# Kernel tuning notes

Measured on AMD Instinct MI355X. Metric: run time of the kernel, lower is better.

Reference implementation:

```python
import jax, jax.numpy as jnp
import numpy as np
from functools import partial

POOL_H, POOL_W = 7, 7


def _bin_index(coord, start, stop, step, n_bins):
    """Map each pixel coordinate to its ROI-pool bin index (or n_bins if outside ROI).

    Bins i < n_bins-1 span [start + i*step, start + (i+1)*step); the last bin
    extends to `stop` (matching the original `(i+1)*h_step if i+1<pool_h else region_h`).
    coord: [L]; start/stop/step: [R] int32. Returns [R, L] int32 in [0, n_bins].
    """
    rel = coord[None, :] - start[:, None]                      # [R, L]
    idx = jnp.minimum(rel // jnp.maximum(step, 1)[:, None], n_bins - 1)
    idx = jnp.where(step[:, None] > 0, idx, n_bins - 1)        # step==0 -> all pixels in last bin
    valid = (rel >= 0) & (coord[None, :] < stop[:, None])
    return jnp.where(valid, idx, n_bins).astype(jnp.int32)


def _roi_pool_image(fm, rois, ph, pw):
    """fm: [H, W, C], rois: [R, 4] relative (h0, w0, h1, w1). Returns [R, ph, pw, C]."""
    H, W, C = fm.shape
    h0 = (H * rois[:, 0]).astype(jnp.int32)   # truncation == tf.cast(..., int32) for >=0
    w0 = (W * rois[:, 1]).astype(jnp.int32)
    h1 = (H * rois[:, 2]).astype(jnp.int32)
    w1 = (W * rois[:, 3]).astype(jnp.int32)
    h_step = (h1 - h0) // ph
    w_step = (w1 - w0) // pw

    idx_h = _bin_index(jnp.arange(H), h0, h1, h_step, ph)      # [R, H]
    idx_w = _bin_index(jnp.arange(W), w0, w1, w_step, pw)      # [R, W]

    neg = jnp.finfo(fm.dtype).min
    fm_whc = jnp.swapaxes(fm, 0, 1)                            # [W, H, C]

    def pool_one(ih, iw):
        # scatter-max columns into width bins (extra slot pw collects out-of-ROI pixels)
        t = jnp.full((pw + 1, H, C), neg, fm.dtype).at[iw].max(fm_whc)[:pw]  # [pw, H, C]
        # scatter-max rows into height bins
        o = jnp.full((ph + 1, pw, C), neg, fm.dtype).at[ih].max(jnp.swapaxes(t, 0, 1))[:ph]
        return o                                               # [ph, pw, C]

    return jax.vmap(pool_one)(idx_h, idx_w)


def setup_inputs() -> dict:
    key = jax.random.key(0)
    k1, k2, k3 = jax.random.split(key, 3)
    feature_map = jax.random.normal(k1, (2, 64, 64, 256), dtype=jnp.float32)
    starts = jax.random.uniform(k2, (2, 256, 2), minval=0.0, maxval=0.3)
    ends = jax.random.uniform(k3, (2, 256, 2), minval=0.6, maxval=1.0)
    rois = jnp.concatenate([starts, ends], axis=-1).astype(jnp.float32)  # (h0, w0, h1, w1)
    return {"feature_map": feature_map, "rois": rois}


def reference(feature_map, rois):
    # per-image ROI max pooling, vmapped over the batch -> [B, R, ph, pw, C]
    pool = partial(_roi_pool_image, ph=POOL_H, pw=POOL_W)
    return jax.vmap(pool)(feature_map, rois)
```

## Files before the change

### kernel.cpp

```cpp
#include <hip/hip_runtime.h>
#include <float.h>

constexpr int H = 64, W = 64, C = 256, PH = 7, PW = 7;

typedef float f32x4 __attribute__((ext_vector_type(4)));

__device__ __forceinline__ f32x4 vmax4(f32x4 a, f32x4 b) {
    f32x4 r;
    r.x = fmaxf(a.x, b.x); r.y = fmaxf(a.y, b.y);
    r.z = fmaxf(a.z, b.z); r.w = fmaxf(a.w, b.w);
    return r;
}

__global__ __launch_bounds__(256) void build_tables(
    const float* __restrict__ fm, float* __restrict__ s4x,
    float* __restrict__ s4y, float* __restrict__ s4xy)
{
    __shared__ f32x4 lds_fm[7][64];
    __shared__ f32x4 lds_sx[7][64];

    const int lane = threadIdx.x & 63;
    const int wave = __builtin_amdgcn_readfirstlane(threadIdx.x >> 6);

    const int x8 = blockIdx.x & 7;
    const int z  = blockIdx.x >> 3;
    const int b  = x8 >> 2;
    const int quart = x8 & 3;
    const int x  = z & (W - 1);
    const int y0 = quart * 16 + ((z >> 6) << 2);

    const int x1 = min(x + 1, W - 1), x2 = min(x + 2, W - 1), x3 = min(x + 3, W - 1);
    const float* fmb = fm + (size_t)b * H * W * C + (size_t)lane * 4;

    #pragma unroll
    for (int s = 0; s < 2; ++s) {
        const int slot = wave + 4 * s;
        if (slot < 7) {
            const int y = min(y0 + slot, H - 1);
            const float* row = fmb + (size_t)y * W * C;
            f32x4 v0 = *(const f32x4*)(row + (size_t)x  * C);
            f32x4 v1 = *(const f32x4*)(row + (size_t)x1 * C);
            f32x4 v2 = *(const f32x4*)(row + (size_t)x2 * C);
            f32x4 v3 = *(const f32x4*)(row + (size_t)x3 * C);
            lds_fm[slot][lane] = v0;
            lds_sx[slot][lane] = vmax4(vmax4(v0, v1), vmax4(v2, v3));
        }
    }
    __syncthreads();

    const int y = y0 + wave;
    const f32x4 sx = lds_sx[wave][lane];
    const f32x4 sy = vmax4(vmax4(lds_fm[wave][lane],     lds_fm[wave + 1][lane]),
                           vmax4(lds_fm[wave + 2][lane], lds_fm[wave + 3][lane]));
    const f32x4 sxy = vmax4(vmax4(lds_sx[wave][lane],     lds_sx[wave + 1][lane]),
                            vmax4(lds_sx[wave + 2][lane], lds_sx[wave + 3][lane]));

    const size_t o = ((size_t)(b * H + y) * W + x) * C + (size_t)lane * 4;
    *(f32x4*)(s4x  + o) = sx;
    *(f32x4*)(s4y  + o) = sy;
    *(f32x4*)(s4xy + o) = sxy;
}

__global__ __launch_bounds__(256) void roi_pool_q(
    const float* __restrict__ fm, const float* __restrict__ rois,
    const float* __restrict__ s4x, const float* __restrict__ s4y,
    const float* __restrict__ s4xy, float* __restrict__ out, int R)
{
    const int lane = threadIdx.x & 63;
    const int wave = __builtin_amdgcn_readfirstlane(threadIdx.x >> 6);

    const int x8 = blockIdx.x & 7;
    const int n  = blockIdx.x >> 3;
    const int b  = x8 >> 2;
    const int g  = x8 & 3;

    int i, id;
    if (g < 3) {
        i  = 2 * g + (n & 1);
        id = (n >> 1) * 4 + wave;
    } else {
        if (n >= 448) return;
        i  = 6;
        id = n * 4 + wave;
    }
    const int r = id / 7;
    const int j = id - 7 * r;

    const float* roi = rois + ((size_t)b * R + r) * 4;
    int h0 = (int)((float)H * roi[0]);
    int w0 = (int)((float)W * roi[1]);
    int h1 = (int)((float)H * roi[2]);
    int w1 = (int)((float)W * roi[3]);
    int hs = (h1 - h0) / PH;
    int ws = (w1 - w0) / PW;

    int ys, ye, xs, xe;
    if (hs > 0) { ys = h0 + i * hs; ye = (i < PH - 1) ? (ys + hs) : h1; }
    else        { ys = h0;          ye = (i == PH - 1) ? h1 : h0; }
    if (ws > 0) { xs = w0 + j * ws; xe = (j < PW - 1) ? (xs + ws) : w1; }
    else        { xs = w0;          xe = (j == PW - 1) ? w1 : w0; }
    ys = __builtin_amdgcn_readfirstlane(max(ys, 0));
    ye = __builtin_amdgcn_readfirstlane(min(ye, H));
    xs = __builtin_amdgcn_readfirstlane(max(xs, 0));
    xe = __builtin_amdgcn_readfirstlane(min(xe, W));

    const int hl = ye - ys, wl = xe - xs;
    const f32x4 NEG = {-FLT_MAX, -FLT_MAX, -FLT_MAX, -FLT_MAX};
    f32x4 a0 = NEG, a1 = NEG, a2 = NEG, a3 = NEG;

    if (hl > 0 && wl > 0) {
        const bool y4 = hl >= 4, x4 = wl >= 4;
        const int ny = y4 ? (hl + 3) >> 2 : hl;
        const int nx = x4 ? (wl + 3) >> 2 : wl;
        const int ystep = y4 ? 4 : 1, xstep = x4 ? 4 : 1;
        const int ycl = y4 ? ye - 4 : ye - 1;
        const int xcl = x4 ? xe - 4 : xe - 1;
        const float* tb = y4 ? (x4 ? s4xy : s4y) : (x4 ? s4x : fm);
        const float* tbb = tb + (size_t)b * H * W * C + lane * 4;

        const int xo0 = min(xs,             xcl) * C;
        const int xo1 = min(xs + xstep,     xcl) * C;
        const int xo2 = min(xs + 2 * xstep, xcl) * C;
        const int xo3 = min(xs + 3 * xstep, xcl) * C;

        #pragma unroll
        for (int ky = 0; ky < 4; ++ky) {
            if (ky < ny) {
                const int y = min(ys + ystep * ky, ycl);
                const float* rowp = tbb + (size_t)y * (W * C);
                a0 = vmax4(a0, *(const f32x4*)(rowp + xo0));
                if (nx > 1) a1 = vmax4(a1, *(const f32x4*)(rowp + xo1));
                if (nx > 2) a2 = vmax4(a2, *(const f32x4*)(rowp + xo2));
                if (nx > 3) a3 = vmax4(a3, *(const f32x4*)(rowp + xo3));
            }
        }
    }
    const f32x4 acc = vmax4(vmax4(a0, a1), vmax4(a2, a3));

    size_t o = ((((size_t)b * R + r) * PH + i) * PW + j) * C + (size_t)lane * 4;
    __builtin_nontemporal_store(acc, reinterpret_cast<f32x4*>(out + o));
}

__global__ __launch_bounds__(256) void roi_pool_direct(
    const float* __restrict__ fm, const float* __restrict__ rois,
    float* __restrict__ out, int R)
{
    const int lane = threadIdx.x & 63;
    const int wave = __builtin_amdgcn_readfirstlane(threadIdx.x >> 6);
    const int b = blockIdx.x & 1;
    int m = (blockIdx.x >> 1) * 4 + wave;
    int j = m % PW; m /= PW;
    int i = m % PH; m /= PH;
    int r = m;

    const float* roi = rois + ((size_t)b * R + r) * 4;
    int h0 = (int)((float)H * roi[0]);
    int w0 = (int)((float)W * roi[1]);
    int h1 = (int)((float)H * roi[2]);
    int w1 = (int)((float)W * roi[3]);
    int hs = (h1 - h0) / PH;
    int ws = (w1 - w0) / PW;

    int ys, ye, xs, xe;
    if (hs > 0) { ys = h0 + i * hs; ye = (i < PH - 1) ? (ys + hs) : h1; }
    else        { ys = h0;          ye = (i == PH - 1) ? h1 : h0; }
    if (ws > 0) { xs = w0 + j * ws; xe = (j < PW - 1) ? (xs + ws) : w1; }
    else        { xs = w0;          xe = (j == PW - 1) ? w1 : w0; }
    ys = __builtin_amdgcn_readfirstlane(max(ys, 0));
    ye = __builtin_amdgcn_readfirstlane(min(ye, H));
    xs = __builtin_amdgcn_readfirstlane(max(xs, 0));
    xe = __builtin_amdgcn_readfirstlane(min(xe, W));

    const f32x4 NEG = {-FLT_MAX, -FLT_MAX, -FLT_MAX, -FLT_MAX};
    f32x4 a0 = NEG, a1 = NEG, a2 = NEG, a3 = NEG;
    const float* fmb = fm + (size_t)b * (H * W * C);
    const int lo = lane * 4;

    for (int y = ys; y < ye; y += 2) {
        const int y1 = min(y + 1, ye - 1);
        const int ro0 = y  * (W * C);
        const int ro1 = y1 * (W * C);
        for (int x = xs; x < xe; x += 2) {
            const int x1 = min(x + 1, xe - 1);
            a0 = vmax4(a0, *(const f32x4*)(fmb + ro0 + x  * C + lo));
            a1 = vmax4(a1, *(const f32x4*)(fmb + ro0 + x1 * C + lo));
            a2 = vmax4(a2, *(const f32x4*)(fmb + ro1 + x  * C + lo));
            a3 = vmax4(a3, *(const f32x4*)(fmb + ro1 + x1 * C + lo));
        }
    }
    f32x4 acc = vmax4(vmax4(a0, a1), vmax4(a2, a3));
    size_t o = ((((size_t)b * R + r) * PH + i) * PW + j) * C + (size_t)lo;
    __builtin_nontemporal_store(acc, reinterpret_cast<f32x4*>(out + o));
}

extern "C" void kernel_launch(void* const* d_in, const int* in_sizes, int n_in,
                              void* d_out, int out_size, void* d_ws, size_t ws_size,
                              hipStream_t stream) {
    const float* fm   = (const float*)d_in[0];
    const float* rois = (const float*)d_in[1];
    float* out = (float*)d_out;

    const int B = in_sizes[0] / (H * W * C);
    const int R = in_sizes[1] / (B * 4);

    const size_t tbl = (size_t)B * H * W * C;
    const size_t need = 3 * tbl * sizeof(float);

    if (B == 2 && R == 256 && ws_size >= need) {
        float* s4x  = (float*)d_ws;
        float* s4y  = s4x + tbl;
        float* s4xy = s4y + tbl;
        build_tables<<<2048, 256, 0, stream>>>(fm, s4x, s4y, s4xy);
        roi_pool_q  <<<7168, 256, 0, stream>>>(fm, rois, s4x, s4y, s4xy, out, R);
    } else {
        const int qblocks = B * (R * PH * PW / 4);
        roi_pool_direct<<<qblocks, 256, 0, stream>>>(fm, rois, out, R);
    }
}
```

Baseline: 24.19 us.

## Build tables from 7x7 LDS tiles and remap pool blocks to exact grid

The table-building kernel now loads a 7x7 tile of feature-map pixels into LDS per block and emits a 4x4 output patch, so neighbouring columns come from LDS instead of repeated global loads. This cuts the block count from 2048 to 512. The ROI pooling kernel uses a flat index mapping over bins, which removes idle blocks and shrinks the grid from 7168 to 6272. The shared gather and bin-bound logic is factored into helpers. The trade-off is larger LDS use per block and more register pressure from holding 14 vectors per thread.

```diff
diff --git a/kernel.cpp b/kernel.cpp
--- a/kernel.cpp
+++ b/kernel.cpp
@@ -16,8 +16,7 @@
     const float* __restrict__ fm, float* __restrict__ s4x,
     float* __restrict__ s4y, float* __restrict__ s4xy)
 {
-    __shared__ f32x4 lds_fm[7][64];
-    __shared__ f32x4 lds_sx[7][64];
+    __shared__ f32x4 lfm[7][7][64];
 
     const int lane = threadIdx.x & 63;
     const int wave = __builtin_amdgcn_readfirstlane(threadIdx.x >> 6);
@@ -26,66 +25,46 @@
     const int z  = blockIdx.x >> 3;
     const int b  = x8 >> 2;
     const int quart = x8 & 3;
-    const int x  = z & (W - 1);
-    const int y0 = quart * 16 + ((z >> 6) << 2);
-
-    const int x1 = min(x + 1, W - 1), x2 = min(x + 2, W - 1), x3 = min(x + 3, W - 1);
+    const int y0 = quart * 16 + ((z >> 4) << 2);
+    const int x0 = (z & 15) << 2;
+
     const float* fmb = fm + (size_t)b * H * W * C + (size_t)lane * 4;
 
+    for (int q = wave; q < 49; q += 4) {
+        const int row = q / 7, col = q % 7;
+        const int y  = min(y0 + row, H - 1);
+        const int xq = min(x0 + col, W - 1);
+        lfm[row][col][lane] = *(const f32x4*)(fmb + ((size_t)y * W + xq) * C);
+    }
+    __syncthreads();
+
+    f32x4 rowv[7], colm[7];
     #pragma unroll
-    for (int s = 0; s < 2; ++s) {
-        const int slot = wave + 4 * s;
-        if (slot < 7) {
-            const int y = min(y0 + slot, H - 1);
-            const float* row = fmb + (size_t)y * W * C;
-            f32x4 v0 = *(const f32x4*)(row + (size_t)x  * C);
-            f32x4 v1 = *(const f32x4*)(row + (size_t)x1 * C);
-            f32x4 v2 = *(const f32x4*)(row + (size_t)x2 * C);
-            f32x4 v3 = *(const f32x4*)(row + (size_t)x3 * C);
-            lds_fm[slot][lane] = v0;
-            lds_sx[slot][lane] = vmax4(vmax4(v0, v1), vmax4(v2, v3));
-        }
-    }
-    __syncthreads();
+    for (int c = 0; c < 7; ++c) {
+        rowv[c] = lfm[wave][c][lane];
+        colm[c] = vmax4(vmax4(rowv[c],            lfm[wave + 1][c][lane]),
+                        vmax4(lfm[wave + 2][c][lane], lfm[wave + 3][c][lane]));
+    }
 
     const int y = y0 + wave;
-    const f32x4 sx = lds_sx[wave][lane];
-    const f32x4 sy = vmax4(vmax4(lds_fm[wave][lane],     lds_fm[wave + 1][lane]),
-                           vmax4(lds_fm[wave + 2][lane], lds_fm[wave + 3][lane]));
-    const f32x4 sxy = vmax4(vmax4(lds_sx[wave][lane],     lds_sx[wave + 1][lane]),
-                            vmax4(lds_sx[wave + 2][lane], lds_sx[wave + 3][lane]));
-
-    const size_t o = ((size_t)(b * H + y) * W + x) * C + (size_t)lane * 4;
-    *(f32x4*)(s4x  + o) = sx;
-    *(f32x4*)(s4y  + o) = sy;
-    *(f32x4*)(s4xy + o) = sxy;
-}
-
-__global__ __launch_bounds__(256) void roi_pool_q(
-    const float* __restrict__ fm, const float* __restrict__ rois,
-    const float* __restrict__ s4x, const float* __restrict__ s4y,
-    const float* __restrict__ s4xy, float* __restrict__ out, int R)
-{
-    const int lane = threadIdx.x & 63;
-    const int wave = __builtin_amdgcn_readfirstlane(threadIdx.x >> 6);
-
-    const int x8 = blockIdx.x & 7;
-    const int n  = blockIdx.x >> 3;
-    const int b  = x8 >> 2;
-    const int g  = x8 & 3;
-
-    int i, id;
-    if (g < 3) {
-        i  = 2 * g + (n & 1);
-        id = (n >> 1) * 4 + wave;
-    } else {
-        if (n >= 448) return;
-        i  = 6;
-        id = n * 4 + wave;
-    }
-    const int r = id / 7;
-    const int j = id - 7 * r;
-
+    #pragma unroll
+    for (int ox = 0; ox < 4; ++ox) {
+        const f32x4 sx  = vmax4(vmax4(rowv[ox], rowv[ox + 1]),
+                                vmax4(rowv[ox + 2], rowv[ox + 3]));
+        const f32x4 sy  = colm[ox];
+        const f32x4 sxy = vmax4(vmax4(colm[ox], colm[ox + 1]),
+                                vmax4(colm[ox + 2], colm[ox + 3]));
+        const size_t o = ((size_t)(b * H + y) * W + (x0 + ox)) * C + (size_t)lane * 4;
+        *(f32x4*)(s4x  + o) = sx;
+        *(f32x4*)(s4y  + o) = sy;
+        *(f32x4*)(s4xy + o) = sxy;
+    }
+}
+
+__device__ __forceinline__ void bin_bounds(
+    const float* __restrict__ rois, int b, int R, int r, int i, int j,
+    int& ys, int& ye, int& xs, int& xe)
+{
     const float* roi = rois + ((size_t)b * R + r) * 4;
     int h0 = (int)((float)H * roi[0]);
     int w0 = (int)((float)W * roi[1]);
@@ -94,7 +73,6 @@
     int hs = (h1 - h0) / PH;
     int ws = (w1 - w0) / PW;
 
-    int ys, ye, xs, xe;
     if (hs > 0) { ys = h0 + i * hs; ye = (i < PH - 1) ? (ys + hs) : h1; }
     else        { ys = h0;          ye = (i == PH - 1) ? h1 : h0; }
     if (ws > 0) { xs = w0 + j * ws; xe = (j < PW - 1) ? (xs + ws) : w1; }
@@ -103,40 +81,87 @@
     ye = __builtin_amdgcn_readfirstlane(min(ye, H));
     xs = __builtin_amdgcn_readfirstlane(max(xs, 0));
     xe = __builtin_amdgcn_readfirstlane(min(xe, W));
-
+}
+
+__device__ __forceinline__ f32x4 gather_bin(
+    int b, int lane, int ys, int ye, int xs, int xe, bool use_tables,
+    const float* __restrict__ fm, const float* __restrict__ s4x,
+    const float* __restrict__ s4y, const float* __restrict__ s4xy)
+{
     const int hl = ye - ys, wl = xe - xs;
     const f32x4 NEG = {-FLT_MAX, -FLT_MAX, -FLT_MAX, -FLT_MAX};
     f32x4 a0 = NEG, a1 = NEG, a2 = NEG, a3 = NEG;
 
     if (hl > 0 && wl > 0) {
-        const bool y4 = hl >= 4, x4 = wl >= 4;
-        const int ny = y4 ? (hl + 3) >> 2 : hl;
-        const int nx = x4 ? (wl + 3) >> 2 : wl;
-        const int ystep = y4 ? 4 : 1, xstep = x4 ? 4 : 1;
-        const int ycl = y4 ? ye - 4 : ye - 1;
-        const int xcl = x4 ? xe - 4 : xe - 1;
-        const float* tb = y4 ? (x4 ? s4xy : s4y) : (x4 ? s4x : fm);
-        const float* tbb = tb + (size_t)b * H * W * C + lane * 4;
-
-        const int xo0 = min(xs,             xcl) * C;
-        const int xo1 = min(xs + xstep,     xcl) * C;
-        const int xo2 = min(xs + 2 * xstep, xcl) * C;
-        const int xo3 = min(xs + 3 * xstep, xcl) * C;
-
-        #pragma unroll
-        for (int ky = 0; ky < 4; ++ky) {
-            if (ky < ny) {
-                const int y = min(ys + ystep * ky, ycl);
-                const float* rowp = tbb + (size_t)y * (W * C);
-                a0 = vmax4(a0, *(const f32x4*)(rowp + xo0));
-                if (nx > 1) a1 = vmax4(a1, *(const f32x4*)(rowp + xo1));
-                if (nx > 2) a2 = vmax4(a2, *(const f32x4*)(rowp + xo2));
-                if (nx > 3) a3 = vmax4(a3, *(const f32x4*)(rowp + xo3));
+        if (use_tables) {
+            const bool y4 = hl >= 4, x4 = wl >= 4;
+            const int ny = y4 ? (hl + 3) >> 2 : hl;
+            const int nx = x4 ? (wl + 3) >> 2 : wl;
+            const int ystep = y4 ? 4 : 1, xstep = x4 ? 4 : 1;
+            const int ycl = y4 ? ye - 4 : ye - 1;
+            const int xcl = x4 ? xe - 4 : xe - 1;
+            const float* tb = y4 ? (x4 ? s4xy : s4y) : (x4 ? s4x : fm);
+            const float* tbb = tb + (size_t)b * H * W * C + lane * 4;
+
+            const int xo0 = min(xs,             xcl) * C;
+            const int xo1 = min(xs + xstep,     xcl) * C;
+            const int xo2 = min(xs + 2 * xstep, xcl) * C;
+            const int xo3 = min(xs + 3 * xstep, xcl) * C;
+
+            #pragma unroll
+            for (int ky = 0; ky < 4; ++ky) {
+                if (ky < ny) {
+                    const int y = min(ys + ystep * ky, ycl);
+                    const float* rowp = tbb + (size_t)y * (W * C);
+                    a0 = vmax4(a0, *(const f32x4*)(rowp + xo0));
+                    if (nx > 1) a1 = vmax4(a1, *(const f32x4*)(rowp + xo1));
+                    if (nx > 2) a2 = vmax4(a2, *(const f32x4*)(rowp + xo2));
+                    if (nx > 3) a3 = vmax4(a3, *(const f32x4*)(rowp + xo3));
+                }
+            }
+        } else {
+            const float* fmb2 = fm + (size_t)b * (H * W * C) + lane * 4;
+            for (int y = ys; y < ye; y += 2) {
+                const int yb = min(y + 1, ye - 1);
+                const int ro0 = y  * (W * C);
+                const int ro1 = yb * (W * C);
+                for (int x = xs; x < xe; x += 2) {
+                    const int xb = min(x + 1, xe - 1);
+                    a0 = vmax4(a0, *(const f32x4*)(fmb2 + ro0 + x  * C));
+                    a1 = vmax4(a1, *(const f32x4*)(fmb2 + ro0 + xb * C));
+                    a2 = vmax4(a2, *(const f32x4*)(fmb2 + ro1 + x  * C));
+                    a3 = vmax4(a3, *(const f32x4*)(fmb2 + ro1 + xb * C));
+                }
             }
         }
     }
-    const f32x4 acc = vmax4(vmax4(a0, a1), vmax4(a2, a3));
-
+    return vmax4(vmax4(a0, a1), vmax4(a2, a3));
+}
+
+__global__ __launch_bounds__(256) void roi_pool_q(
+    const float* __restrict__ fm, const float* __restrict__ rois,
+    const float* __restrict__ s4x, const float* __restrict__ s4y,
+    const float* __restrict__ s4xy, float* __restrict__ out, int R)
+{
+    const int lane = threadIdx.x & 63;
+    const int wave = __builtin_amdgcn_readfirstlane(threadIdx.x >> 6);
+
+    const int x8 = blockIdx.x & 7;
+    const int n  = blockIdx.x >> 3;
+    const int b  = x8 >> 2;
+    const int c  = x8 & 3;
+
+    const int t  = c * 784 + n;
+    const int i  = t / 448;
+    const int m  = t - 448 * i;
+    const int id = m * 4 + wave;
+    const int r  = id / 7;
+    const int j  = id - 7 * r;
+
+    int ys, ye, xs, xe;
+    bin_bounds(rois, b, R, r, i, j, ys, ye, xs, xe);
+    const f32x4 acc = gather_bin(b, lane, ys, ye, xs, xe, true,
+                                 fm, s4x, s4y, s4xy);
     size_t o = ((((size_t)b * R + r) * PH + i) * PW + j) * C + (size_t)lane * 4;
     __builtin_nontemporal_store(acc, reinterpret_cast<f32x4*>(out + o));
 }
@@ -153,43 +178,11 @@
     int i = m % PH; m /= PH;
     int r = m;
 
-    const float* roi = rois + ((size_t)b * R + r) * 4;
-    int h0 = (int)((float)H * roi[0]);
-    int w0 = (int)((float)W * roi[1]);
-    int h1 = (int)((float)H * roi[2]);
-    int w1 = (int)((float)W * roi[3]);
-    int hs = (h1 - h0) / PH;
-    int ws = (w1 - w0) / PW;
-
     int ys, ye, xs, xe;
-    if (hs > 0) { ys = h0 + i * hs; ye = (i < PH - 1) ? (ys + hs) : h1; }
-    else        { ys = h0;          ye = (i == PH - 1) ? h1 : h0; }
-    if (ws > 0) { xs = w0 + j * ws; xe = (j < PW - 1) ? (xs + ws) : w1; }
-    else        { xs = w0;          xe = (j == PW - 1) ? w1 : w0; }
-    ys = __builtin_amdgcn_readfirstlane(max(ys, 0));
-    ye = __builtin_amdgcn_readfirstlane(min(ye, H));
-    xs = __builtin_amdgcn_readfirstlane(max(xs, 0));
-    xe = __builtin_amdgcn_readfirstlane(min(xe, W));
-
-    const f32x4 NEG = {-FLT_MAX, -FLT_MAX, -FLT_MAX, -FLT_MAX};
-    f32x4 a0 = NEG, a1 = NEG, a2 = NEG, a3 = NEG;
-    const float* fmb = fm + (size_t)b * (H * W * C);
-    const int lo = lane * 4;
-
-    for (int y = ys; y < ye; y += 2) {
-        const int y1 = min(y + 1, ye - 1);
-        const int ro0 = y  * (W * C);
-        const int ro1 = y1 * (W * C);
-        for (int x = xs; x < xe; x += 2) {
-            const int x1 = min(x + 1, xe - 1);
-            a0 = vmax4(a0, *(const f32x4*)(fmb + ro0 + x  * C + lo));
-            a1 = vmax4(a1, *(const f32x4*)(fmb + ro0 + x1 * C + lo));
-            a2 = vmax4(a2, *(const f32x4*)(fmb + ro1 + x  * C + lo));
-            a3 = vmax4(a3, *(const f32x4*)(fmb + ro1 + x1 * C + lo));
-        }
-    }
-    f32x4 acc = vmax4(vmax4(a0, a1), vmax4(a2, a3));
-    size_t o = ((((size_t)b * R + r) * PH + i) * PW + j) * C + (size_t)lo;
+    bin_bounds(rois, b, R, r, i, j, ys, ye, xs, xe);
+    const f32x4 acc = gather_bin(b, lane, ys, ye, xs, xe, false,
+                                 fm, nullptr, nullptr, nullptr);
+    size_t o = ((((size_t)b * R + r) * PH + i) * PW + j) * C + (size_t)lane * 4;
     __builtin_nontemporal_store(acc, reinterpret_cast<f32x4*>(out + o));
 }
 
@@ -210,8 +203,8 @@
         float* s4x  = (float*)d_ws;
         float* s4y  = s4x + tbl;
         float* s4xy = s4y + tbl;
-        build_tables<<<2048, 256, 0, stream>>>(fm, s4x, s4y, s4xy);
-        roi_pool_q  <<<7168, 256, 0, stream>>>(fm, rois, s4x, s4y, s4xy, out, R);
+        build_tables<<<512,  256, 0, stream>>>(fm, s4x, s4y, s4xy);
+        roi_pool_q  <<<6272, 256, 0, stream>>>(fm, rois, s4x, s4y, s4xy, out, R);
     } else {
         const int qblocks = B * (R * PH * PW / 4);
         roi_pool_direct<<<qblocks, 256, 0, stream>>>(fm, rois, out, R);
```

New measurement: 26.19 us. 1.08x slower.
